# Optimization experiments

Hardware: AMD Instinct MI355X
Metric: run time of the kernel (lower is better)

## Reference

```python
import jax, jax.numpy as jnp
import numpy as np

B, C, H, W = 16, 384, 64, 64
NUM_POS = 48        # (7*7 - 1) offsets, origin excluded
STRIDE = 16
K = 3               # LO_kernel_size
SIGMA = 0.5         # LO_sigma


def setup_inputs() -> dict:
    key = jax.random.key(0)
    k1, k2 = jax.random.split(key)
    inp = jax.random.normal(k1, (B, C, H, W), dtype=jnp.float32)
    # init_offset: grid (iw*stride, ih*stride), skipping origin (use_origin=False)
    offs = []
    for ih in range(-3, 4):
        for iw in range(-3, 4):
            if ih == 0 and iw == 0:
                continue
            offs.append((iw * STRIDE, ih * STRIDE))
    offset = jnp.asarray(np.array(offs, dtype=np.float32))
    # small fractional perturbation so the learnable-offset gaussian path is non-trivial
    offset = offset + jax.random.uniform(k2, (NUM_POS, 2), minval=-0.45, maxval=0.45)
    return {"inp": inp, "offset": offset}


def _displace(inp, shift):
    """Integer per-channel-group spatial shift with zero padding.
    out[b,g,c,y,x] = inp[b,g,c, y - oy[g], x - ox[g]] (content moves by +offset).
    shift: [G,2] int32, (x, y) order as in the torch module.
    """
    b, c, h, w = inp.shape
    g = shift.shape[0]
    cpp = c // g
    x5 = inp.reshape(b, g, cpp, h, w)
    ox, oy = shift[:, 0], shift[:, 1]
    ys = jnp.arange(h, dtype=jnp.int32)[None, :] - oy[:, None]   # [G,H]
    xs = jnp.arange(w, dtype=jnp.int32)[None, :] - ox[:, None]   # [G,W]
    ymask = (ys >= 0) & (ys < h)
    xmask = (xs >= 0) & (xs < w)
    ysc = jnp.clip(ys, 0, h - 1)
    xsc = jnp.clip(xs, 0, w - 1)
    gth = jnp.take_along_axis(x5, ysc[None, :, None, :, None], axis=3)
    gth = jnp.take_along_axis(gth, xsc[None, :, None, None, :], axis=4)
    mask = (ymask[None, :, None, :, None] & xmask[None, :, None, None, :]).astype(inp.dtype)
    return (gth * mask).reshape(b, c, h, w)


def reference(inp, offset):
    b, c, h, w = inp.shape
    g = offset.shape[0]
    cpp = c // g
    # DisplaceCUDA uses offset.detach().round(): integer shift, no grad through it
    rnd = jax.lax.stop_gradient(jnp.round(offset))
    out = _displace(inp, rnd.astype(jnp.int32))
    # gaussian_translate: depthwise conv with gaussian kernel centered at
    # fractional part (offset - round(offset)); grads flow through this path only.
    frac = offset - rnd                                  # [G,2]
    r = jnp.arange(K, dtype=inp.dtype) - (K // 2)
    dx = r[None, None, :] + frac[:, 0, None, None]       # x varies along kernel width
    dy = r[None, :, None] + frac[:, 1, None, None]       # y varies along kernel height
    kern = jnp.exp(-(dx * dx + dy * dy) / (2.0 * SIGMA ** 2))   # [G,K,K]
    kern = kern / jnp.sum(kern, axis=(1, 2), keepdims=True)
    kern_full = jnp.repeat(kern, cpp, axis=0)[:, None]   # [C,1,K,K]
    out_LO = jax.lax.conv_general_dilated(
        out, kern_full, window_strides=(1, 1),
        padding=[(K // 2, K // 2), (K // 2, K // 2)],
        dimension_numbers=("NCHW", "OIHW", "NCHW"),
        feature_group_count=c)
    return out, out_LO
```

## Files before the change

### kernel.cpp

```cpp
#include <hip/hip_runtime.h>

#define B_   16
#define C_   384
#define H_   64
#define W_   64
#define G_   48
#define CPP_ 8
#define PLANE (H_ * W_)
#define INV_2SIG2 2.0f

#define SROWS 66
#define SCOLS 67

__global__ __launch_bounds__(256) void displace_fused_kernel(
    const float* __restrict__ inp,
    const float* __restrict__ offset,
    float* __restrict__ out0,
    float* __restrict__ out1)
{
    __shared__ float s[SROWS * SCOLS];
    __shared__ float wk[9];
    __shared__ int   shv[2];

    const int p = blockIdx.x;
    const int c = p % C_;
    const int g = c >> 3;

    if (threadIdx.x == 0) {
        const float ofx = offset[2 * g + 0];
        const float ofy = offset[2 * g + 1];
        const float rx = rintf(ofx);
        const float ry = rintf(ofy);
        const float fx = ofx - rx;
        const float fy = ofy - ry;
        float wtmp[9];
        float sum = 0.0f;
        #pragma unroll
        for (int i = 0; i < 3; ++i) {
            const float dy = (float)(i - 1) + fy;
            #pragma unroll
            for (int j = 0; j < 3; ++j) {
                const float dx = (float)(j - 1) + fx;
                const float v = __expf(-(dx * dx + dy * dy) * INV_2SIG2);
                wtmp[i * 3 + j] = v;
                sum += v;
            }
        }
        const float inv = 1.0f / sum;
        #pragma unroll
        for (int k = 0; k < 9; ++k) wk[k] = wtmp[k] * inv;
        shv[0] = (int)rx;
        shv[1] = (int)ry;
    }

    for (int i = threadIdx.x; i < SROWS * SCOLS; i += 256) s[i] = 0.0f;
    __syncthreads();

    const int ox = shv[0];
    const int oy = shv[1];
    const float* plane = inp + (size_t)p * PLANE;

    for (int idx = threadIdx.x; idx < PLANE; idx += 256) {
        const int y = idx >> 6;
        const int x = idx & 63;
        const int sy = y - oy;
        const int sx = x - ox;
        float v = 0.0f;
        if ((unsigned)sy < (unsigned)H_ && (unsigned)sx < (unsigned)W_)
            v = plane[sy * W_ + sx];
        s[(y + 1) * SCOLS + (x + 1)] = v;
    }
    __syncthreads();

    float* o0 = out0 + (size_t)p * PLANE;
    float* o1 = out1 + (size_t)p * PLANE;
    const float w0 = wk[0], w1 = wk[1], w2 = wk[2];
    const float w3 = wk[3], w4 = wk[4], w5 = wk[5];
    const float w6 = wk[6], w7 = wk[7], w8 = wk[8];

    for (int idx = threadIdx.x; idx < PLANE; idx += 256) {
        const int y = idx >> 6;
        const int x = idx & 63;
        const float* r0 = &s[y * SCOLS + x];
        const float* r1 = r0 + SCOLS;
        const float* r2 = r1 + SCOLS;
        float a;
        a  = r0[0] * w0 + r0[1] * w1 + r0[2] * w2;
        a += r1[0] * w3 + r1[1] * w4 + r1[2] * w5;
        a += r2[0] * w6 + r2[1] * w7 + r2[2] * w8;
        o0[idx] = r1[1];
        o1[idx] = a;
    }
}

extern "C" void kernel_launch(void* const* d_in, const int* in_sizes, int n_in,
                              void* d_out, int out_size, void* d_ws, size_t ws_size,
                              hipStream_t stream) {
    const float* inp    = (const float*)d_in[0];
    const float* offset = (const float*)d_in[1];
    float* out0 = (float*)d_out;
    float* out1 = out0 + (size_t)B_ * C_ * PLANE;
    displace_fused_kernel<<<B_ * C_, 256, 0, stream>>>(inp, offset, out0, out1);
}
```

Before: 282.6 us.

## Vectorize stores, batch loads, compute weights per thread, zero only halo

Each thread now computes the Gaussian weights and integer shift itself, removing the single-thread setup and its shared-memory handoff. Only the halo border of the shared tile is zeroed. All 16 rows of global loads per thread are issued before the shared stores, giving more memory parallelism. The output pass computes four adjacent pixels per thread and writes them as float4 for both outputs, at the cost of more registers and some shared-memory bank conflicts from the strided row reads.

```diff
diff --git a/kernel.cpp b/kernel.cpp
--- a/kernel.cpp
+++ b/kernel.cpp
@@ -4,13 +4,9 @@
 #define C_   384
 #define H_   64
 #define W_   64
-#define G_   48
-#define CPP_ 8
 #define PLANE (H_ * W_)
-#define INV_2SIG2 2.0f
-
+#define SCOLS 67
 #define SROWS 66
-#define SCOLS 67
 
 __global__ __launch_bounds__(256) void displace_fused_kernel(
     const float* __restrict__ inp,
@@ -19,21 +15,22 @@
     float* __restrict__ out1)
 {
     __shared__ float s[SROWS * SCOLS];
-    __shared__ float wk[9];
-    __shared__ int   shv[2];
 
-    const int p = blockIdx.x;
-    const int c = p % C_;
-    const int g = c >> 3;
+    const int tid = threadIdx.x;
+    const int p   = blockIdx.x;
+    const int g   = (p % C_) >> 3;
 
-    if (threadIdx.x == 0) {
-        const float ofx = offset[2 * g + 0];
-        const float ofy = offset[2 * g + 1];
-        const float rx = rintf(ofx);
-        const float ry = rintf(ofy);
-        const float fx = ofx - rx;
-        const float fy = ofy - ry;
-        float wtmp[9];
+    const float ofx = offset[2 * g + 0];
+    const float ofy = offset[2 * g + 1];
+    const float rx = rintf(ofx);
+    const float ry = rintf(ofy);
+    const float fx = ofx - rx;
+    const float fy = ofy - ry;
+    const int ox = (int)rx;
+    const int oy = (int)ry;
+
+    float w[9];
+    {
         float sum = 0.0f;
         #pragma unroll
         for (int i = 0; i < 3; ++i) {
@@ -41,55 +38,73 @@
             #pragma unroll
             for (int j = 0; j < 3; ++j) {
                 const float dx = (float)(j - 1) + fx;
-                const float v = __expf(-(dx * dx + dy * dy) * INV_2SIG2);
-                wtmp[i * 3 + j] = v;
+                const float v = __expf(-(dx * dx + dy * dy) * 2.0f);
+                w[i * 3 + j] = v;
                 sum += v;
             }
         }
         const float inv = 1.0f / sum;
         #pragma unroll
-        for (int k = 0; k < 9; ++k) wk[k] = wtmp[k] * inv;
-        shv[0] = (int)rx;
-        shv[1] = (int)ry;
+        for (int k = 0; k < 9; ++k) w[k] *= inv;
     }
 
-    for (int i = threadIdx.x; i < SROWS * SCOLS; i += 256) s[i] = 0.0f;
-    __syncthreads();
+    if (tid < 67) { s[tid] = 0.0f; s[65 * SCOLS + tid] = 0.0f; }
+    if (tid < 64) { s[(tid + 1) * SCOLS] = 0.0f; s[(tid + 1) * SCOLS + 65] = 0.0f; }
 
-    const int ox = shv[0];
-    const int oy = shv[1];
-    const float* plane = inp + (size_t)p * PLANE;
+    const float* __restrict__ plane = inp + (size_t)p * PLANE;
+    const int lane = tid & 63;
+    const int wv   = tid >> 6;
+    const int sx   = lane - ox;
+    const bool vx  = (unsigned)sx < (unsigned)W_;
 
-    for (int idx = threadIdx.x; idx < PLANE; idx += 256) {
-        const int y = idx >> 6;
-        const int x = idx & 63;
+    float v[16];
+    #pragma unroll
+    for (int k = 0; k < 16; ++k) {
+        const int y  = (k << 2) + wv;
         const int sy = y - oy;
-        const int sx = x - ox;
-        float v = 0.0f;
-        if ((unsigned)sy < (unsigned)H_ && (unsigned)sx < (unsigned)W_)
-            v = plane[sy * W_ + sx];
-        s[(y + 1) * SCOLS + (x + 1)] = v;
+        v[k] = (vx && (unsigned)sy < (unsigned)H_) ? plane[sy * W_ + sx] : 0.0f;
+    }
+    #pragma unroll
+    for (int k = 0; k < 16; ++k) {
+        const int y = (k << 2) + wv;
+        s[(y + 1) * SCOLS + 1 + lane] = v[k];
     }
     __syncthreads();
 
-    float* o0 = out0 + (size_t)p * PLANE;
-    float* o1 = out1 + (size_t)p * PLANE;
-    const float w0 = wk[0], w1 = wk[1], w2 = wk[2];
-    const float w3 = wk[3], w4 = wk[4], w5 = wk[5];
-    const float w6 = wk[6], w7 = wk[7], w8 = wk[8];
+    float* __restrict__ o0 = out0 + (size_t)p * PLANE;
+    float* __restrict__ o1 = out1 + (size_t)p * PLANE;
 
-    for (int idx = threadIdx.x; idx < PLANE; idx += 256) {
-        const int y = idx >> 6;
-        const int x = idx & 63;
+    #pragma unroll
+    for (int it = 0; it < 4; ++it) {
+        const int base = it * 1024 + tid * 4;
+        const int y = base >> 6;
+        const int x = base & 63;
         const float* r0 = &s[y * SCOLS + x];
         const float* r1 = r0 + SCOLS;
         const float* r2 = r1 + SCOLS;
-        float a;
-        a  = r0[0] * w0 + r0[1] * w1 + r0[2] * w2;
-        a += r1[0] * w3 + r1[1] * w4 + r1[2] * w5;
-        a += r2[0] * w6 + r2[1] * w7 + r2[2] * w8;
-        o0[idx] = r1[1];
-        o1[idx] = a;
+
+        float p0[6], p1[6], p2[6];
+        #pragma unroll
+        for (int j = 0; j < 6; ++j) { p0[j] = r0[j]; p1[j] = r1[j]; p2[j] = r2[j]; }
+
+        const float4 d0 = make_float4(p1[1], p1[2], p1[3], p1[4]);
+
+        float a0, a1, a2, a3;
+        a0 = p0[0]*w[0] + p0[1]*w[1] + p0[2]*w[2]
+           + p1[0]*w[3] + p1[1]*w[4] + p1[2]*w[5]
+           + p2[0]*w[6] + p2[1]*w[7] + p2[2]*w[8];
+        a1 = p0[1]*w[0] + p0[2]*w[1] + p0[3]*w[2]
+           + p1[1]*w[3] + p1[2]*w[4] + p1[3]*w[5]
+           + p2[1]*w[6] + p2[2]*w[7] + p2[3]*w[8];
+        a2 = p0[2]*w[0] + p0[3]*w[1] + p0[4]*w[2]
+           + p1[2]*w[3] + p1[3]*w[4] + p1[4]*w[5]
+           + p2[2]*w[6] + p2[3]*w[7] + p2[4]*w[8];
+        a3 = p0[3]*w[0] + p0[4]*w[1] + p0[5]*w[2]
+           + p1[3]*w[3] + p1[4]*w[4] + p1[5]*w[5]
+           + p2[3]*w[6] + p2[4]*w[7] + p2[5]*w[8];
+
+        *(float4*)(o0 + base) = d0;
+        *(float4*)(o1 + base) = make_float4(a0, a1, a2, a3);
     }
 }
 
```

Measured after the change: 269.1 us. -4.8%, faster.
